# Performance work log

Hardware: AMD Instinct MI355X
Metric: run time of the kernel (lower is better)

Reference implementation:

```python
import jax, jax.numpy as jnp
import numpy as np


def _gla_forward(hidden_state, Wq, bq, Wk, bk, Wv, bv, Wg, bg, Wo, bo):
    # hidden_state: (B, T, H)
    q = hidden_state @ Wq + bq                       # (B, T, K)
    k = jax.nn.sigmoid(hidden_state @ Wk + bk)       # (B, T, K)
    g = jax.nn.sigmoid(hidden_state @ Wg + bg)       # (B, T, K)
    v = hidden_state @ Wv + bv                       # (B, T, V)

    B = hidden_state.shape[0]
    K = Wq.shape[1]
    V = Wv.shape[1]
    state0 = jnp.zeros((B, K, V), dtype=hidden_state.dtype)

    def step(state, inp):
        q_t, k_t, g_t, v_t = inp                     # (B,K),(B,K),(B,K),(B,V)
        # state = state * gate[..., None] + k outer v
        state = state * g_t[:, :, None] + k_t[:, :, None] * v_t[:, None, :]
        out_t = jnp.einsum('bkv,bk->bv', state, q_t)  # (B, V)
        return state, out_t

    # scan over time: move T to leading axis
    xs = (jnp.swapaxes(q, 0, 1), jnp.swapaxes(k, 0, 1),
          jnp.swapaxes(g, 0, 1), jnp.swapaxes(v, 0, 1))
    final_state, outs = jax.lax.scan(step, state0, xs)  # outs: (T, B, V)
    out = jnp.swapaxes(outs, 0, 1)                      # (B, T, V)
    out = out @ Wo + bo                                 # (B, T, O)
    return out, final_state


def setup_inputs() -> dict:
    key = jax.random.key(0)
    ks = jax.random.split(key, 12)
    B, T, H, K, V, O = 8, 2048, 1024, 256, 256, 1024
    s = 0.02
    return {
        'hidden_state': jax.random.normal(ks[0], (B, T, H), dtype=jnp.float32),
        'Wq': jax.random.normal(ks[1], (H, K), dtype=jnp.float32) * s,
        'bq': jax.random.normal(ks[2], (K,), dtype=jnp.float32) * s,
        'Wk': jax.random.normal(ks[3], (H, K), dtype=jnp.float32) * s,
        'bk': jax.random.normal(ks[4], (K,), dtype=jnp.float32) * s,
        'Wv': jax.random.normal(ks[5], (H, V), dtype=jnp.float32) * s,
        'bv': jax.random.normal(ks[6], (V,), dtype=jnp.float32) * s,
        'Wg': jax.random.normal(ks[7], (H, K), dtype=jnp.float32) * s,
        'bg': jax.random.normal(ks[8], (K,), dtype=jnp.float32) * s,
        'Wo': jax.random.normal(ks[9], (V, O), dtype=jnp.float32) * s,
        'bo': jax.random.normal(ks[10], (O,), dtype=jnp.float32) * s,
    }


def reference(hidden_state, Wq, bq, Wk, bk, Wv, bv, Wg, bg, Wo, bo):
    return _gla_forward(hidden_state, Wq, bq, Wk, bk, Wv, bv, Wg, bg, Wo, bo)
```

## Files before the change

kernel.cpp:

```cpp
#include <hip/hip_runtime.h>

#define Bb 8
#define Tt 2048
#define Hh 1024
#define Kk 256
#define Vv 256
#define Oo 1024
#define CC 64
#define NC 32

typedef __attribute__((ext_vector_type(8))) __bf16 bf16x8;
typedef __attribute__((ext_vector_type(4))) float f32x4;

__device__ __forceinline__ unsigned short f2b(float f) {
  unsigned u = __float_as_uint(f);
  u = (u + 0x7FFFu + ((u >> 16) & 1u)) >> 16;
  return (unsigned short)u;
}
__device__ __forceinline__ float b2f(unsigned short u) {
  return __uint_as_float(((unsigned)u) << 16);
}
__device__ __forceinline__ void gload_lds16(const unsigned short* g, unsigned short* l) {
  __builtin_amdgcn_global_load_lds(
      (const __attribute__((address_space(1))) void*)g,
      (__attribute__((address_space(3))) void*)l, 16, 0, 0);
}

__global__ __launch_bounds__(256) void cast_bf16_kernel(const float* __restrict__ in,
                                                        unsigned short* __restrict__ out,
                                                        int n4) {
  int i = blockIdx.x * 256 + threadIdx.x;
  if (i >= n4) return;
  float4 v = ((const float4*)in)[i];
  ushort4 o;
  o.x = f2b(v.x); o.y = f2b(v.y); o.z = f2b(v.z); o.w = f2b(v.w);
  ((ushort4*)out)[i] = o;
}

__global__ __launch_bounds__(256) void transpose_cast_kernel(const float* __restrict__ W,
                                                             unsigned short* __restrict__ WT,
                                                             int H, int N) {
  __shared__ float tile[32][33];
  int h0 = blockIdx.x * 32, n0 = blockIdx.y * 32;
  int tx = threadIdx.x & 31, ty = threadIdx.x >> 5;
  for (int r = ty; r < 32; r += 8)
    tile[r][tx] = W[(size_t)(h0 + r) * N + n0 + tx];
  __syncthreads();
  for (int r = ty; r < 32; r += 8)
    WT[(size_t)(n0 + r) * H + h0 + tx] = f2b(tile[tx][r]);
}

#define BM 128
#define BN 128
#define BK 64

template <int MODE>
__global__ __launch_bounds__(256, 4) void gemm_mf_kernel(
    const unsigned short* __restrict__ A, const unsigned short* __restrict__ Bt,
    const float* __restrict__ b0p, const float* __restrict__ b1p,
    const float* __restrict__ b2p, const float* __restrict__ b3p,
    float* __restrict__ Cf,
    unsigned short* __restrict__ O0, unsigned short* __restrict__ O1,
    unsigned short* __restrict__ O2, unsigned short* __restrict__ O3,
    int M, int N, int K) {
  __shared__ __align__(16) unsigned short shbuf[16384];
  unsigned short* As = shbuf;
  unsigned short* Bs = shbuf + 8192;
  const int tid = threadIdx.x;
  const int lane = tid & 63, wid = tid >> 6;
  const int wm = wid >> 1, wn = wid & 1;
  const int lin = blockIdx.x + blockIdx.y * gridDim.x;
  const int xcd = lin & 7;
  const int jj = lin >> 3;
  const int mpg = gridDim.y >> 3;
  const int m0 = (xcd * mpg + jj / gridDim.x) * BM;
  const int n0 = (jj % gridDim.x) * BN;
  const int fr = lane & 15, fq = lane >> 4;
  const int srl = lane >> 3;
  const int scs = ((lane & 7) ^ srl) * 8;
  const unsigned short* gaBase = A + (size_t)(m0 + srl) * K + scs;
  const unsigned short* gbBase = Bt + (size_t)(n0 + srl) * K + scs;

  f32x4 acc[4][4] = {};
  const int nt = K / BK;
  for (int t = 0; t < nt; ++t) {
    const int k0 = t * BK;
    __syncthreads();
#pragma unroll
    for (int inst = 0; inst < 4; ++inst) {
      const int rb = wid * 32 + inst * 8;
      gload_lds16(gaBase + (size_t)rb * K + k0, &As[rb * BK]);
      gload_lds16(gbBase + (size_t)rb * K + k0, &Bs[rb * BK]);
    }
    __syncthreads();
#pragma unroll
    for (int ks = 0; ks < 2; ++ks) {
      bf16x8 af[4], bfv[4];
#pragma unroll
      for (int j = 0; j < 4; ++j) {
        const int R = wn * 64 + j * 16 + fr;
        const int ch = ((ks << 2) | fq) ^ (fr & 7);
        bfv[j] = *(const bf16x8*)&Bs[R * BK + ch * 8];
      }
#pragma unroll
      for (int i = 0; i < 4; ++i) {
        const int R = wm * 64 + i * 16 + fr;
        const int ch = ((ks << 2) | fq) ^ (fr & 7);
        af[i] = *(const bf16x8*)&As[R * BK + ch * 8];
      }
#pragma unroll
      for (int i = 0; i < 4; ++i)
#pragma unroll
        for (int j = 0; j < 4; ++j)
          acc[i][j] = __builtin_amdgcn_mfma_f32_16x16x32_bf16(af[i], bfv[j], acc[i][j], 0, 0, 0);
    }
  }
  if (MODE == 1) {
#pragma unroll
    for (int j = 0; j < 4; ++j) {
      const int n = n0 + wn * 64 + j * 16 + fr;
      const float bv = b0p[n];
#pragma unroll
      for (int i = 0; i < 4; ++i) {
        const int mb = m0 + wm * 64 + i * 16 + fq * 4;
#pragma unroll
        for (int r = 0; r < 4; ++r)
          Cf[(size_t)(mb + r) * N + n] = acc[i][j][r] + bv;
      }
    }
  } else {
    __syncthreads();
    const int sel = n0 >> 8;
    const float* bp = sel == 0 ? b0p : sel == 1 ? b1p : sel == 2 ? b2p : b3p;
#pragma unroll
    for (int j = 0; j < 4; ++j) {
      const int ncol = wn * 64 + j * 16 + fr;
      const int nloc = (n0 & 255) + ncol;
      const float bv = bp[nloc];
#pragma unroll
      for (int i = 0; i < 4; ++i) {
#pragma unroll
        for (int r = 0; r < 4; ++r) {
          const int ml = wm * 64 + i * 16 + fq * 4 + r;
          const float x = acc[i][j][r] + bv;
          unsigned short us;
          if (sel == 0) {
            us = f2b(x);
          } else if (sel == 1) {
            us = f2b(1.f / (1.f + expf(-x)));
          } else if (sel == 2) {
            float e = exp2f(-x * 1.44269504f);
            float lg = -log2f(1.f + e);
            _Float16 hv = (_Float16)lg;
            __builtin_memcpy(&us, &hv, 2);
          } else {
            us = f2b(x);
          }
          if (sel == 3) {
            const int cm = (ml >> 3) ^ (ncol & 15);
            shbuf[ncol * 128 + cm * 8 + (ml & 7)] = us;
          } else {
            const int cn = (ncol >> 3) ^ (ml & 15);
            shbuf[ml * 128 + cn * 8 + (ncol & 7)] = us;
          }
        }
      }
    }
    __syncthreads();
    const int row = tid >> 1;
    const int half = tid & 1;
    if (sel == 3) {
      unsigned short* dst = O3 + ((size_t)(m0 >> 11) * Vv + (n0 & 255) + row) * Tt +
                            (m0 & 2047) + half * 64;
#pragma unroll
      for (int ic = 0; ic < 8; ++ic) {
        const int chunk = half * 8 + ic;
        const int sc = chunk ^ (row & 15);
        *(uint4*)(dst + ic * 8) = *(const uint4*)&shbuf[row * 128 + sc * 8];
      }
    } else {
      unsigned short* Op = sel == 0 ? O0 : sel == 1 ? O1 : O2;
      unsigned short* dst = Op + (size_t)(m0 + row) * 256 + (n0 & 255) + half * 64;
#pragma unroll
      for (int ic = 0; ic < 8; ++ic) {
        const int chunk = half * 8 + ic;
        const int sc = chunk ^ (row & 15);
        *(uint4*)(dst + ic * 8) = *(const uint4*)&shbuf[row * 128 + sc * 8];
      }
    }
  }
}

__global__ __launch_bounds__(256) void prep_sgemm_kernel(
    const unsigned short* __restrict__ qb, const unsigned short* __restrict__ kb,
    const unsigned short* __restrict__ lgb, const unsigned short* __restrict__ vTb,
    unsigned short* __restrict__ q2b, unsigned short* __restrict__ qab,
    unsigned short* __restrict__ kab,
    float* __restrict__ LBb, float* __restrict__ Dendb,
    unsigned short* __restrict__ Sb) {
  __shared__ __align__(16) unsigned short khs[256][72];
  const int c = blockIdx.x, b = blockIdx.y;
  const int k = threadIdx.x;
  const int task = b * NC + c;
  const size_t rowbase = ((size_t)b * Tt + (size_t)c * CC) * Kk + k;
  float Ls = 0.f;
  float LBr[4];
#pragma unroll
  for (int gq = 0; gq < 4; ++gq) {
    LBr[gq] = Ls;
#pragma unroll
    for (int tt = 0; tt < 16; ++tt) {
      int t = gq * 16 + tt;
      _Float16 hv;
      __builtin_memcpy(&hv, &lgb[rowbase + (size_t)t * Kk], 2);
      Ls += (float)hv;
    }
  }
  const float Lend = Ls;
#pragma unroll
  for (int gq = 0; gq < 4; ++gq) LBb[(size_t)task * 1024 + gq * 256 + k] = LBr[gq];
  Dendb[task * 256 + k] = exp2f(Lend);
  float L = 0.f;
#pragma unroll
  for (int gq = 0; gq < 4; ++gq) {
    const float LBc = LBr[gq];
    unsigned kw[8];
#pragma unroll
    for (int tt = 0; tt < 16; ++tt) {
      int t = gq * 16 + tt;
      size_t off = rowbase + (size_t)t * Kk;
      _Float16 hv;
      __builtin_memcpy(&hv, &lgb[off], 2);
      L += (float)hv;
      float qv = b2f(qb[off]);
      float kv = b2f(kb[off]);
      q2b[off] = f2b(qv * exp2f(L));
      qab[off] = f2b(qv * exp2f(L - LBc));
      kab[off] = f2b(kv * exp2f(LBc - L));
      unsigned short kh = f2b(kv * exp2f(Lend - L));
      if (tt & 1) kw[tt >> 1] |= ((unsigned)kh) << 16;
      else        kw[tt >> 1] = kh;
    }
    uint4 u0; u0.x = kw[0]; u0.y = kw[1]; u0.z = kw[2]; u0.w = kw[3];
    uint4 u1; u1.x = kw[4]; u1.y = kw[5]; u1.z = kw[6]; u1.w = kw[7];
    *(uint4*)&khs[k][gq * 16] = u0;
    *(uint4*)&khs[k][gq * 16 + 8] = u1;
  }
  __syncthreads();
  const int tid = threadIdx.x, lane = tid & 63, w = tid >> 6;
  const int fr = lane & 15, fq = lane >> 4, fk = fq * 8;
  const unsigned short* vt = vTb + (size_t)b * (Vv * Tt) + (size_t)c * CC;
  for (int vb4 = 0; vb4 < 4; ++vb4) {
    f32x4 acc[4][4] = {};
#pragma unroll
    for (int ks = 0; ks < 2; ++ks) {
      bf16x8 af[4], bf[4];
#pragma unroll
      for (int i = 0; i < 4; ++i)
        af[i] = *(const bf16x8*)&khs[w * 64 + i * 16 + fr][ks * 32 + fk];
#pragma unroll
      for (int j = 0; j < 4; ++j)
        bf[j] = *(const bf16x8*)(vt + (size_t)(vb4 * 64 + j * 16 + fr) * Tt + ks * 32 + fk);
#pragma unroll
      for (int i = 0; i < 4; ++i)
#pragma unroll
        for (int j = 0; j < 4; ++j)
          acc[i][j] = __builtin_amdgcn_mfma_f32_16x16x32_bf16(af[i], bf[j], acc[i][j], 0, 0, 0);
    }
#pragma unroll
    for (int i = 0; i < 4; ++i)
#pragma unroll
      for (int j = 0; j < 4; ++j)
#pragma unroll
        for (int r = 0; r < 4; ++r)
          Sb[(size_t)task * (Kk * Vv) + (size_t)(w * 64 + i * 16 + fq * 4 + r) * Vv +
             vb4 * 64 + j * 16 + fr] = f2b(acc[i][j][r]);
  }
}

__global__ __launch_bounds__(256) void passR_kernel(
    const unsigned short* __restrict__ Sb, const float* __restrict__ Dendb,
    unsigned short* __restrict__ S0Tb, float* __restrict__ state_out) {
  const int vt = blockIdx.x, kt = blockIdx.y, b = blockIdx.z;
  const int tid = threadIdx.x;
  const int kq = tid >> 2;
  const int vq = tid & 3;
  const int vr = tid >> 3;
  const int kqq = tid & 7;
  __shared__ __align__(16) unsigned short Ts[32][72];
  float st[8];
#pragma unroll
  for (int j = 0; j < 8; ++j) st[j] = 0.f;
  for (int c = 0; c < NC; ++c) {
    const int task = b * NC + c;
#pragma unroll
    for (int j = 0; j < 8; ++j) Ts[vq * 8 + j][kq] = f2b(st[j]);
    __syncthreads();
    {
      unsigned short* dst = S0Tb + (size_t)task * (Kk * Vv) +
                            (size_t)(vt * 32 + vr) * Kk + kt * 64 + kqq * 8;
      *(uint4*)dst = *(const uint4*)&Ts[vr][kqq * 8];
    }
    __syncthreads();
    const float d = Dendb[task * 256 + kt * 64 + kq];
    const unsigned short* sp = Sb + (size_t)task * (Kk * Vv) +
                               (size_t)(kt * 64 + kq) * Vv + vt * 32 + vq * 8;
    uint4 raw = *(const uint4*)sp;
    unsigned ws_[4] = {raw.x, raw.y, raw.z, raw.w};
#pragma unroll
    for (int e = 0; e < 4; ++e) {
      float lo = __uint_as_float(ws_[e] << 16);
      float hi = __uint_as_float(ws_[e] & 0xFFFF0000u);
      st[e * 2]     = d * st[e * 2] + lo;
      st[e * 2 + 1] = d * st[e * 2 + 1] + hi;
    }
  }
  float* so = state_out + (size_t)(b * Kk + kt * 64 + kq) * Vv + vt * 32 + vq * 8;
#pragma unroll
  for (int j = 0; j < 8; ++j) so[j] = st[j];
}

__global__ __launch_bounds__(256) void passO_kernel(
    const unsigned short* __restrict__ qab, const unsigned short* __restrict__ kab,
    const unsigned short* __restrict__ q2b, const float* __restrict__ LBb,
    const unsigned short* __restrict__ S0Tb, const unsigned short* __restrict__ vTb,
    unsigned short* __restrict__ attb) {
  const int c = blockIdx.x, b = blockIdx.y;
  const int task = b * NC + c;
  const int tid = threadIdx.x, lane = tid & 63, w = tid >> 6;
  const int fr = lane & 15, fq = lane >> 4, fk = fq * 8;
  __shared__ float LB_s[4][256];
  __shared__ float D_s[6][256];
  __shared__ __align__(16) unsigned short A_s[64][72];
  const size_t tbase = (size_t)task * (CC * Kk);
  for (int idx = tid; idx < 1024; idx += 256) LB_s[idx >> 8][idx & 255] = LBb[(size_t)task * 1024 + idx];
  for (int idx = tid; idx < 64 * 72 / 2; idx += 256) ((unsigned*)A_s)[idx] = 0;
  __syncthreads();
  {
    const int kk = tid;
#pragma unroll
    for (int pi = 0; pi < 6; ++pi) {
      const int I = (pi >= 3) ? 3 : (pi >= 1) ? 2 : 1;
      const int J = pi - (I * (I - 1)) / 2;
      D_s[pi][kk] = exp2f(LB_s[I][kk] - LB_s[J][kk]);
    }
  }
  __syncthreads();
  for (int p = w; p < 10; p += 4) {
    const int I = (p >= 6) ? 3 : (p >= 3) ? 2 : (p >= 1) ? 1 : 0;
    const int J = p - (I * (I + 1)) / 2;
    const int pidx = (I * (I - 1)) / 2 + J;
    f32x4 acc = {0.f, 0.f, 0.f, 0.f};
#pragma unroll
    for (int ks = 0; ks < 8; ++ks) {
      const int k0 = ks * 32 + fk;
      bf16x8 af = *(const bf16x8*)(qab + tbase + (size_t)(I * 16 + fr) * Kk + k0);
      if (I != J) {
#pragma unroll
        for (int e = 0; e < 8; ++e)
          af[e] = (__bf16)((float)af[e] * D_s[pidx][k0 + e]);
      }
      bf16x8 bf = *(const bf16x8*)(kab + tbase + (size_t)(J * 16 + fr) * Kk + k0);
      acc = __builtin_amdgcn_mfma_f32_16x16x32_bf16(af, bf, acc, 0, 0, 0);
    }
#pragma unroll
    for (int r = 0; r < 4; ++r) {
      const int ml = fq * 4 + r, nl = fr;
      bool keep = (I != J) || (nl <= ml);
      A_s[I * 16 + ml][J * 16 + nl] = keep ? f2b(acc[r]) : (unsigned short)0;
    }
  }
  __syncthreads();
  f32x4 acc2[4][4] = {};
  const unsigned short* q2t = q2b + tbase;
  const unsigned short* s0t = S0Tb + (size_t)task * (Kk * Vv);
  const unsigned short* vtp = vTb + (size_t)b * (Vv * Tt) + (size_t)c * CC;
  const int vbase = w * 64;
#pragma unroll
  for (int ks = 0; ks < 8; ++ks) {
    const int k0 = ks * 32 + fk;
    bf16x8 af[4], bf[4];
#pragma unroll
    for (int i = 0; i < 4; ++i) af[i] = *(const bf16x8*)(q2t + (size_t)(i * 16 + fr) * Kk + k0);
#pragma unroll
    for (int j = 0; j < 4; ++j) bf[j] = *(const bf16x8*)(s0t + (size_t)(vbase + j * 16 + fr) * Kk + k0);
#pragma unroll
    for (int i = 0; i < 4; ++i)
#pragma unroll
      for (int j = 0; j < 4; ++j)
        acc2[i][j] = __builtin_amdgcn_mfma_f32_16x16x32_bf16(af[i], bf[j], acc2[i][j], 0, 0, 0);
  }
#pragma unroll
  for (int ks = 0; ks < 2; ++ks) {
    const int s0 = ks * 32 + fk;
    bf16x8 af[4], bf[4];
#pragma unroll
    for (int i = 0; i < 4; ++i) af[i] = *(const bf16x8*)&A_s[i * 16 + fr][s0];
#pragma unroll
    for (int j = 0; j < 4; ++j) bf[j] = *(const bf16x8*)(vtp + (size_t)(vbase + j * 16 + fr) * Tt + s0);
#pragma unroll
    for (int i = 0; i < 4; ++i)
#pragma unroll
      for (int j = 0; j < 4; ++j)
        acc2[i][j] = __builtin_amdgcn_mfma_f32_16x16x32_bf16(af[i], bf[j], acc2[i][j], 0, 0, 0);
  }
#pragma unroll
  for (int i = 0; i < 4; ++i)
#pragma unroll
    for (int j = 0; j < 4; ++j)
#pragma unroll
      for (int r = 0; r < 4; ++r)
        attb[((size_t)b * Tt + c * CC + i * 16 + fq * 4 + r) * Vv + vbase + j * 16 + fr]
            = f2b(acc2[i][j][r]);
}

extern "C" void kernel_launch(void* const* d_in, const int* in_sizes, int n_in,
                              void* d_out, int out_size, void* d_ws, size_t ws_size,
                              hipStream_t stream) {
  const float* hs = (const float*)d_in[0];
  const float* Wq = (const float*)d_in[1];
  const float* bq = (const float*)d_in[2];
  const float* Wk = (const float*)d_in[3];
  const float* bk = (const float*)d_in[4];
  const float* Wv = (const float*)d_in[5];
  const float* bv = (const float*)d_in[6];
  const float* Wg = (const float*)d_in[7];
  const float* bg = (const float*)d_in[8];
  const float* Wo = (const float*)d_in[9];
  const float* bo = (const float*)d_in[10];

  float* out = (float*)d_out;
  float* state_out = out + (size_t)Bb * Tt * Oo;

  char* p = (char*)d_ws;
  auto alloc = [&](size_t bytes) {
    char* r = p;
    p += (bytes + 255) & ~(size_t)255;
    return r;
  };
  unsigned short* hsb   = (unsigned short*)alloc((size_t)Bb * Tt * Hh * 2);
  unsigned short* WallT = (unsigned short*)alloc((size_t)1024 * Hh * 2);
  unsigned short* WoT   = (unsigned short*)alloc((size_t)Oo * Vv * 2);
  unsigned short* qb    = (unsigned short*)alloc((size_t)Bb * Tt * Kk * 2);
  unsigned short* kb    = (unsigned short*)alloc((size_t)Bb * Tt * Kk * 2);
  unsigned short* lgb   = (unsigned short*)alloc((size_t)Bb * Tt * Kk * 2);
  unsigned short* vTb   = (unsigned short*)alloc((size_t)Bb * Vv * Tt * 2);
  unsigned short* attb  = (unsigned short*)alloc((size_t)Bb * Tt * Vv * 2);
  unsigned short* q2b   = (unsigned short*)alloc((size_t)Bb * Tt * Kk * 2);
  unsigned short* qab   = (unsigned short*)alloc((size_t)Bb * Tt * Kk * 2);
  unsigned short* kab   = (unsigned short*)alloc((size_t)Bb * Tt * Kk * 2);
  float*          LBb   = (float*)alloc((size_t)Bb * NC * 4 * Kk * 4);
  float*          Dendb = (float*)alloc((size_t)Bb * NC * Kk * 4);
  unsigned short* Sb    = (unsigned short*)alloc((size_t)Bb * NC * Kk * Vv * 2);
  unsigned short* S0Tb  = (unsigned short*)alloc((size_t)Bb * NC * Kk * Vv * 2);

  int n4 = Bb * Tt * Hh / 4;
  cast_bf16_kernel<<<(n4 + 255) / 256, 256, 0, stream>>>(hs, hsb, n4);
  transpose_cast_kernel<<<dim3(Hh / 32, Kk / 32), 256, 0, stream>>>(Wq, WallT + 0 * Kk * Hh, Hh, Kk);
  transpose_cast_kernel<<<dim3(Hh / 32, Kk / 32), 256, 0, stream>>>(Wk, WallT + 1 * Kk * Hh, Hh, Kk);
  transpose_cast_kernel<<<dim3(Hh / 32, Kk / 32), 256, 0, stream>>>(Wg, WallT + 2 * Kk * Hh, Hh, Kk);
  transpose_cast_kernel<<<dim3(Hh / 32, Kk / 32), 256, 0, stream>>>(Wv, WallT + 3 * Kk * Hh, Hh, Kk);
  transpose_cast_kernel<<<dim3(Vv / 32, Oo / 32), 256, 0, stream>>>(Wo, WoT, Vv, Oo);

  gemm_mf_kernel<0><<<dim3(1024 / BN, (Bb * Tt) / BM), 256, 0, stream>>>(
      hsb, WallT, bq, bk, bg, bv, nullptr, qb, kb, lgb, vTb, Bb * Tt, 1024, Hh);

  prep_sgemm_kernel<<<dim3(NC, Bb), 256, 0, stream>>>(qb, kb, lgb, vTb, q2b, qab, kab,
                                                      LBb, Dendb, Sb);

  passR_kernel<<<dim3(Vv / 32, Kk / 64, Bb), 256, 0, stream>>>(Sb, Dendb, S0Tb, state_out);

  passO_kernel<<<dim3(NC, Bb), 256, 0, stream>>>(qab, kab, q2b, LBb, S0Tb, vTb, attb);

  gemm_mf_kernel<1><<<dim3(Oo / BN, (Bb * Tt) / BM), 256, 0, stream>>>(
      attb, WoT, bo, nullptr, nullptr, nullptr, out, nullptr, nullptr, nullptr, nullptr,
      Bb * Tt, Oo, Vv);
}
```

Baseline: 218.5 us.

## Fuse output projection GEMM into passO kernel, dropping attb buffer

The output projection (att @ Wo + bo) now runs inside passO. The attention tile is kept in shared memory and multiplied by WoT with MFMA, and the fp32 result is written directly. This removes the intermediate attb global buffer and a separate GEMM launch. In exchange, the projection runs on only 256 blocks, WoT is read from global memory without LDS staging, and the output stores use a column-strided pattern.

New measurement: 222.8 us. Within noise of the previous version (+2.0%).

```diff
diff --git a/kernel.cpp b/kernel.cpp
--- a/kernel.cpp
+++ b/kernel.cpp
@@ -54,12 +54,10 @@
 #define BN 128
 #define BK 64
 
-template <int MODE>
-__global__ __launch_bounds__(256, 4) void gemm_mf_kernel(
+__global__ __launch_bounds__(256, 4) void gemm_proj_kernel(
     const unsigned short* __restrict__ A, const unsigned short* __restrict__ Bt,
     const float* __restrict__ b0p, const float* __restrict__ b1p,
     const float* __restrict__ b2p, const float* __restrict__ b3p,
-    float* __restrict__ Cf,
     unsigned short* __restrict__ O0, unsigned short* __restrict__ O1,
     unsigned short* __restrict__ O2, unsigned short* __restrict__ O3,
     int M, int N, int K) {
@@ -115,78 +113,62 @@
           acc[i][j] = __builtin_amdgcn_mfma_f32_16x16x32_bf16(af[i], bfv[j], acc[i][j], 0, 0, 0);
     }
   }
-  if (MODE == 1) {
-#pragma unroll
-    for (int j = 0; j < 4; ++j) {
-      const int n = n0 + wn * 64 + j * 16 + fr;
-      const float bv = b0p[n];
-#pragma unroll
-      for (int i = 0; i < 4; ++i) {
-        const int mb = m0 + wm * 64 + i * 16 + fq * 4;
-#pragma unroll
-        for (int r = 0; r < 4; ++r)
-          Cf[(size_t)(mb + r) * N + n] = acc[i][j][r] + bv;
-      }
-    }
-  } else {
-    __syncthreads();
-    const int sel = n0 >> 8;
-    const float* bp = sel == 0 ? b0p : sel == 1 ? b1p : sel == 2 ? b2p : b3p;
-#pragma unroll
-    for (int j = 0; j < 4; ++j) {
-      const int ncol = wn * 64 + j * 16 + fr;
-      const int nloc = (n0 & 255) + ncol;
-      const float bv = bp[nloc];
-#pragma unroll
-      for (int i = 0; i < 4; ++i) {
-#pragma unroll
-        for (int r = 0; r < 4; ++r) {
-          const int ml = wm * 64 + i * 16 + fq * 4 + r;
-          const float x = acc[i][j][r] + bv;
-          unsigned short us;
-          if (sel == 0) {
-            us = f2b(x);
-          } else if (sel == 1) {
-            us = f2b(1.f / (1.f + expf(-x)));
-          } else if (sel == 2) {
-            float e = exp2f(-x * 1.44269504f);
-            float lg = -log2f(1.f + e);
-            _Float16 hv = (_Float16)lg;
-            __builtin_memcpy(&us, &hv, 2);
-          } else {
-            us = f2b(x);
-          }
-          if (sel == 3) {
-            const int cm = (ml >> 3) ^ (ncol & 15);
-            shbuf[ncol * 128 + cm * 8 + (ml & 7)] = us;
-          } else {
-            const int cn = (ncol >> 3) ^ (ml & 15);
-            shbuf[ml * 128 + cn * 8 + (ncol & 7)] = us;
-          }
+  __syncthreads();
+  const int sel = n0 >> 8;
+  const float* bp = sel == 0 ? b0p : sel == 1 ? b1p : sel == 2 ? b2p : b3p;
+#pragma unroll
+  for (int j = 0; j < 4; ++j) {
+    const int ncol = wn * 64 + j * 16 + fr;
+    const float bv = bp[(n0 & 255) + ncol];
+#pragma unroll
+    for (int i = 0; i < 4; ++i) {
+#pragma unroll
+      for (int r = 0; r < 4; ++r) {
+        const int ml = wm * 64 + i * 16 + fq * 4 + r;
+        const float x = acc[i][j][r] + bv;
+        unsigned short us;
+        if (sel == 0) {
+          us = f2b(x);
+        } else if (sel == 1) {
+          us = f2b(1.f / (1.f + expf(-x)));
+        } else if (sel == 2) {
+          float e = exp2f(-x * 1.44269504f);
+          float lg = -log2f(1.f + e);
+          _Float16 hv = (_Float16)lg;
+          __builtin_memcpy(&us, &hv, 2);
+        } else {
+          us = f2b(x);
+        }
+        if (sel == 3) {
+          const int cm = (ml >> 3) ^ (ncol & 15);
+          shbuf[ncol * 128 + cm * 8 + (ml & 7)] = us;
+        } else {
+          const int cn = (ncol >> 3) ^ (ml & 15);
+          shbuf[ml * 128 + cn * 8 + (ncol & 7)] = us;
         }
       }
     }
-    __syncthreads();
-    const int row = tid >> 1;
-    const int half = tid & 1;
-    if (sel == 3) {
-      unsigned short* dst = O3 + ((size_t)(m0 >> 11) * Vv + (n0 & 255) + row) * Tt +
-                            (m0 & 2047) + half * 64;
-#pragma unroll
-      for (int ic = 0; ic < 8; ++ic) {
-        const int chunk = half * 8 + ic;
-        const int sc = chunk ^ (row & 15);
-        *(uint4*)(dst + ic * 8) = *(const uint4*)&shbuf[row * 128 + sc * 8];
-      }
-    } else {
-      unsigned short* Op = sel == 0 ? O0 : sel == 1 ? O1 : O2;
-      unsigned short* dst = Op + (size_t)(m0 + row) * 256 + (n0 & 255) + half * 64;
-#pragma unroll
-      for (int ic = 0; ic < 8; ++ic) {
-        const int chunk = half * 8 + ic;
-        const int sc = chunk ^ (row & 15);
-        *(uint4*)(dst + ic * 8) = *(const uint4*)&shbuf[row * 128 + sc * 8];
-      }
+  }
+  __syncthreads();
+  const int row = tid >> 1;
+  const int half = tid & 1;
+  if (sel == 3) {
+    unsigned short* dst = O3 + ((size_t)(m0 >> 11) * Vv + (n0 & 255) + row) * Tt +
+                          (m0 & 2047) + half * 64;
+#pragma unroll
+    for (int ic = 0; ic < 8; ++ic) {
+      const int chunk = half * 8 + ic;
+      const int sc = chunk ^ (row & 15);
+      *(uint4*)(dst + ic * 8) = *(const uint4*)&shbuf[row * 128 + sc * 8];
+    }
+  } else {
+    unsigned short* Op = sel == 0 ? O0 : sel == 1 ? O1 : O2;
+    unsigned short* dst = Op + (size_t)(m0 + row) * 256 + (n0 & 255) + half * 64;
+#pragma unroll
+    for (int ic = 0; ic < 8; ++ic) {
+      const int chunk = half * 8 + ic;
+      const int sc = chunk ^ (row & 15);
+      *(uint4*)(dst + ic * 8) = *(const uint4*)&shbuf[row * 128 + sc * 8];
     }
   }
 }
@@ -324,7 +306,8 @@
     const unsigned short* __restrict__ qab, const unsigned short* __restrict__ kab,
     const unsigned short* __restrict__ q2b, const float* __restrict__ LBb,
     const unsigned short* __restrict__ S0Tb, const unsigned short* __restrict__ vTb,
-    unsigned short* __restrict__ attb) {
+    const unsigned short* __restrict__ WoT, const float* __restrict__ bo,
+    float* __restrict__ outp) {
   const int c = blockIdx.x, b = blockIdx.y;
   const int task = b * NC + c;
   const int tid = threadIdx.x, lane = tid & 63, w = tid >> 6;
@@ -332,6 +315,7 @@
   __shared__ float LB_s[4][256];
   __shared__ float D_s[6][256];
   __shared__ __align__(16) unsigned short A_s[64][72];
+  __shared__ __align__(16) unsigned short att_s[64][264];
   const size_t tbase = (size_t)task * (CC * Kk);
   for (int idx = tid; idx < 1024; idx += 256) LB_s[idx >> 8][idx & 255] = LBb[(size_t)task * 1024 + idx];
   for (int idx = tid; idx < 64 * 72 / 2; idx += 256) ((unsigned*)A_s)[idx] = 0;
@@ -410,8 +394,40 @@
     for (int j = 0; j < 4; ++j)
 #pragma unroll
       for (int r = 0; r < 4; ++r)
-        attb[((size_t)b * Tt + c * CC + i * 16 + fq * 4 + r) * Vv + vbase + j * 16 + fr]
-            = f2b(acc2[i][j][r]);
+        att_s[i * 16 + fq * 4 + r][vbase + j * 16 + fr] = f2b(acc2[i][j][r]);
+  __syncthreads();
+  const size_t orow = (size_t)b * Tt + (size_t)c * CC;
+  for (int cc = 0; cc < 4; ++cc) {
+    const int o0 = w * 256 + cc * 64;
+    f32x4 acc3[4][4] = {};
+#pragma unroll
+    for (int ks = 0; ks < 8; ++ks) {
+      const int k0 = ks * 32 + fk;
+      bf16x8 af[4], bf[4];
+#pragma unroll
+      for (int i = 0; i < 4; ++i)
+        af[i] = *(const bf16x8*)&att_s[i * 16 + fr][k0];
+#pragma unroll
+      for (int j = 0; j < 4; ++j)
+        bf[j] = *(const bf16x8*)(WoT + (size_t)(o0 + j * 16 + fr) * Vv + k0);
+#pragma unroll
+      for (int i = 0; i < 4; ++i)
+#pragma unroll
+        for (int j = 0; j < 4; ++j)
+          acc3[i][j] = __builtin_amdgcn_mfma_f32_16x16x32_bf16(af[i], bf[j], acc3[i][j], 0, 0, 0);
+    }
+#pragma unroll
+    for (int j = 0; j < 4; ++j) {
+      const int o = o0 + j * 16 + fr;
+      const float bv = bo[o];
+#pragma unroll
+      for (int i = 0; i < 4; ++i) {
+#pragma unroll
+        for (int r = 0; r < 4; ++r)
+          outp[(orow + i * 16 + fq * 4 + r) * Oo + o] = acc3[i][j][r] + bv;
+      }
+    }
+  }
 }
 
 extern "C" void kernel_launch(void* const* d_in, const int* in_sizes, int n_in,
@@ -445,7 +461,6 @@
   unsigned short* kb    = (unsigned short*)alloc((size_t)Bb * Tt * Kk * 2);
   unsigned short* lgb   = (unsigned short*)alloc((size_t)Bb * Tt * Kk * 2);
   unsigned short* vTb   = (unsigned short*)alloc((size_t)Bb * Vv * Tt * 2);
-  unsigned short* attb  = (unsigned short*)alloc((size_t)Bb * Tt * Vv * 2);
   unsigned short* q2b   = (unsigned short*)alloc((size_t)Bb * Tt * Kk * 2);
   unsigned short* qab   = (unsigned short*)alloc((size_t)Bb * Tt * Kk * 2);
   unsigned short* kab   = (unsigned short*)alloc((size_t)Bb * Tt * Kk * 2);
@@ -462,17 +477,14 @@
   transpose_cast_kernel<<<dim3(Hh / 32, Kk / 32), 256, 0, stream>>>(Wv, WallT + 3 * Kk * Hh, Hh, Kk);
   transpose_cast_kernel<<<dim3(Vv / 32, Oo / 32), 256, 0, stream>>>(Wo, WoT, Vv, Oo);
 
-  gemm_mf_kernel<0><<<dim3(1024 / BN, (Bb * Tt) / BM), 256, 0, stream>>>(
-      hsb, WallT, bq, bk, bg, bv, nullptr, qb, kb, lgb, vTb, Bb * Tt, 1024, Hh);
+  gemm_proj_kernel<<<dim3(1024 / BN, (Bb * Tt) / BM), 256, 0, stream>>>(
+      hsb, WallT, bq, bk, bg, bv, qb, kb, lgb, vTb, Bb * Tt, 1024, Hh);
 
   prep_sgemm_kernel<<<dim3(NC, Bb), 256, 0, stream>>>(qb, kb, lgb, vTb, q2b, qab, kab,
                                                       LBb, Dendb, Sb);
 
   passR_kernel<<<dim3(Vv / 32, Kk / 64, Bb), 256, 0, stream>>>(Sb, Dendb, S0Tb, state_out);
 
-  passO_kernel<<<dim3(NC, Bb), 256, 0, stream>>>(qab, kab, q2b, LBb, S0Tb, vTb, attb);
-
-  gemm_mf_kernel<1><<<dim3(Oo / BN, (Bb * Tt) / BM), 256, 0, stream>>>(
-      attb, WoT, bo, nullptr, nullptr, nullptr, out, nullptr, nullptr, nullptr, nullptr,
-      Bb * Tt, Oo, Vv);
-}
+  passO_kernel<<<dim3(NC, Bb), 256, 0, stream>>>(qab, kab, q2b, LBb, S0Tb, vTb,
+                                                 WoT, bo, out);
+}
```

## Load GEMM MFMA fragments directly from global memory, bypassing LDS staging

Applied to the files above, without the earlier changes.

Replaces the LDS-staged tile loop (global_load_lds into swizzled shared tiles plus two barriers per k-step) with each wave loading its bf16x8 MFMA fragments straight from global memory into registers. This removes the barriers and LDS traffic, but gives up sharing: every wave now fetches its own A and B rows, so the two waves that use the same rows each load them, relying on L1/L2 to absorb the duplicates. The per-lane loads are 16-byte strided rows and may coalesce less well, and the shared buffer is still declared but unused.

New measurement: 324.7 us. 1.49x slower.

```diff
diff --git a/kernel.cpp b/kernel.cpp
--- a/kernel.cpp
+++ b/kernel.cpp
@@ -19,11 +19,6 @@
 }
 __device__ __forceinline__ float b2f(unsigned short u) {
   return __uint_as_float(((unsigned)u) << 16);
-}
-__device__ __forceinline__ void gload_lds16(const unsigned short* g, unsigned short* l) {
-  __builtin_amdgcn_global_load_lds(
-      (const __attribute__((address_space(1))) void*)g,
-      (__attribute__((address_space(3))) void*)l, 16, 0, 0);
 }
 
 __global__ __launch_bounds__(256) void cast_bf16_kernel(const float* __restrict__ in,
@@ -52,10 +47,9 @@
 
 #define BM 128
 #define BN 128
-#define BK 64
 
 template <int MODE>
-__global__ __launch_bounds__(256, 4) void gemm_mf_kernel(
+__global__ __launch_bounds__(256, 4) void gemm_dir_kernel(
     const unsigned short* __restrict__ A, const unsigned short* __restrict__ Bt,
     const float* __restrict__ b0p, const float* __restrict__ b1p,
     const float* __restrict__ b2p, const float* __restrict__ b3p,
@@ -64,8 +58,6 @@
     unsigned short* __restrict__ O2, unsigned short* __restrict__ O3,
     int M, int N, int K) {
   __shared__ __align__(16) unsigned short shbuf[16384];
-  unsigned short* As = shbuf;
-  unsigned short* Bs = shbuf + 8192;
   const int tid = threadIdx.x;
   const int lane = tid & 63, wid = tid >> 6;
   const int wm = wid >> 1, wn = wid & 1;
@@ -76,45 +68,26 @@
   const int m0 = (xcd * mpg + jj / gridDim.x) * BM;
   const int n0 = (jj % gridDim.x) * BN;
   const int fr = lane & 15, fq = lane >> 4;
-  const int srl = lane >> 3;
-  const int scs = ((lane & 7) ^ srl) * 8;
-  const unsigned short* gaBase = A + (size_t)(m0 + srl) * K + scs;
-  const unsigned short* gbBase = Bt + (size_t)(n0 + srl) * K + scs;
+  const unsigned short* aBase = A + (size_t)(m0 + wm * 64 + fr) * K + fq * 8;
+  const unsigned short* bBase = Bt + (size_t)(n0 + wn * 64 + fr) * K + fq * 8;
 
   f32x4 acc[4][4] = {};
-  const int nt = K / BK;
-  for (int t = 0; t < nt; ++t) {
-    const int k0 = t * BK;
-    __syncthreads();
-#pragma unroll
-    for (int inst = 0; inst < 4; ++inst) {
-      const int rb = wid * 32 + inst * 8;
-      gload_lds16(gaBase + (size_t)rb * K + k0, &As[rb * BK]);
-      gload_lds16(gbBase + (size_t)rb * K + k0, &Bs[rb * BK]);
-    }
-    __syncthreads();
-#pragma unroll
-    for (int ks = 0; ks < 2; ++ks) {
-      bf16x8 af[4], bfv[4];
-#pragma unroll
-      for (int j = 0; j < 4; ++j) {
-        const int R = wn * 64 + j * 16 + fr;
-        const int ch = ((ks << 2) | fq) ^ (fr & 7);
-        bfv[j] = *(const bf16x8*)&Bs[R * BK + ch * 8];
-      }
-#pragma unroll
-      for (int i = 0; i < 4; ++i) {
-        const int R = wm * 64 + i * 16 + fr;
-        const int ch = ((ks << 2) | fq) ^ (fr & 7);
-        af[i] = *(const bf16x8*)&As[R * BK + ch * 8];
-      }
-#pragma unroll
-      for (int i = 0; i < 4; ++i)
-#pragma unroll
-        for (int j = 0; j < 4; ++j)
-          acc[i][j] = __builtin_amdgcn_mfma_f32_16x16x32_bf16(af[i], bfv[j], acc[i][j], 0, 0, 0);
-    }
-  }
+#pragma unroll 2
+  for (int k0 = 0; k0 < K; k0 += 32) {
+    bf16x8 af[4], bfv[4];
+#pragma unroll
+    for (int i = 0; i < 4; ++i)
+      af[i] = *(const bf16x8*)(aBase + (size_t)(i * 16) * K + k0);
+#pragma unroll
+    for (int j = 0; j < 4; ++j)
+      bfv[j] = *(const bf16x8*)(bBase + (size_t)(j * 16) * K + k0);
+#pragma unroll
+    for (int i = 0; i < 4; ++i)
+#pragma unroll
+      for (int j = 0; j < 4; ++j)
+        acc[i][j] = __builtin_amdgcn_mfma_f32_16x16x32_bf16(af[i], bfv[j], acc[i][j], 0, 0, 0);
+  }
+
   if (MODE == 1) {
 #pragma unroll
     for (int j = 0; j < 4; ++j) {
@@ -129,14 +102,12 @@
       }
     }
   } else {
-    __syncthreads();
     const int sel = n0 >> 8;
     const float* bp = sel == 0 ? b0p : sel == 1 ? b1p : sel == 2 ? b2p : b3p;
 #pragma unroll
     for (int j = 0; j < 4; ++j) {
       const int ncol = wn * 64 + j * 16 + fr;
-      const int nloc = (n0 & 255) + ncol;
-      const float bv = bp[nloc];
+      const float bv = bp[(n0 & 255) + ncol];
 #pragma unroll
       for (int i = 0; i < 4; ++i) {
 #pragma unroll
@@ -462,7 +433,7 @@
   transpose_cast_kernel<<<dim3(Hh / 32, Kk / 32), 256, 0, stream>>>(Wv, WallT + 3 * Kk * Hh, Hh, Kk);
   transpose_cast_kernel<<<dim3(Vv / 32, Oo / 32), 256, 0, stream>>>(Wo, WoT, Vv, Oo);
 
-  gemm_mf_kernel<0><<<dim3(1024 / BN, (Bb * Tt) / BM), 256, 0, stream>>>(
+  gemm_dir_kernel<0><<<dim3(1024 / BN, (Bb * Tt) / BM), 256, 0, stream>>>(
       hsb, WallT, bq, bk, bg, bv, nullptr, qb, kb, lgb, vTb, Bb * Tt, 1024, Hh);
 
   prep_sgemm_kernel<<<dim3(NC, Bb), 256, 0, stream>>>(qb, kb, lgb, vTb, q2b, qab, kab,
@@ -472,7 +443,7 @@
 
   passO_kernel<<<dim3(NC, Bb), 256, 0, stream>>>(qab, kab, q2b, LBb, S0Tb, vTb, attb);
 
-  gemm_mf_kernel<1><<<dim3(Oo / BN, (Bb * Tt) / BM), 256, 0, stream>>>(
+  gemm_dir_kernel<1><<<dim3(Oo / BN, (Bb * Tt) / BM), 256, 0, stream>>>(
       attb, WoT, bo, nullptr, nullptr, nullptr, out, nullptr, nullptr, nullptr, nullptr,
       Bb * Tt, Oo, Vv);
 }
```
